# Optimization experiments

Measured on AMD Instinct MI355X. Metric: run time of the kernel, lower is better.

Reference implementation:

```python
import jax, jax.numpy as jnp
import numpy as np

HID = 1024
HEADS = 16
HEAD_DIM = HID // HEADS
FFN = 4096
EPS = 1e-5


def setup_inputs() -> dict:
    key = jax.random.key(0)
    ks = jax.random.split(key, 12)
    s = lambda k, shape, fan_in: jax.random.normal(k, shape, jnp.float32) * (fan_in ** -0.5)
    return {
        "hidden_states": jax.random.normal(ks[0], (2, 2048, HID), jnp.float32),
        "Wq": s(ks[1], (HID, HID), HID),
        "Wk": s(ks[2], (HID, HID), HID),
        "Wv": s(ks[3], (HID, HID), HID),
        "Wo": s(ks[4], (HID, HID), HID),
        "W1": s(ks[5], (HID, FFN), HID),
        "b1": jnp.zeros((FFN,), jnp.float32),
        "W2": s(ks[6], (FFN, HID), FFN),
        "b2": jnp.zeros((HID,), jnp.float32),
        "ln1_scale": jnp.ones((HID,), jnp.float32),
        "ln1_shift": jnp.zeros((HID,), jnp.float32),
        "ln2_scale": jnp.ones((HID,), jnp.float32),
        "ln2_shift": jnp.zeros((HID,), jnp.float32),
    }


def _layer_norm(x, scale, shift):
    mean = jnp.mean(x, axis=-1, keepdims=True)
    var = jnp.var(x, axis=-1, keepdims=True)  # biased, matches unbiased=False
    return (x - mean) * jax.lax.rsqrt(var + EPS) * scale + shift


def _forward(hidden_states, Wq, Wk, Wv, Wo, W1, b1, W2, b2,
             ln1_scale, ln1_shift, ln2_scale, ln2_shift):
    bsz, seq_len, _ = hidden_states.shape
    residual = hidden_states
    x = _layer_norm(hidden_states, ln1_scale, ln1_shift)

    # q/k/v projections -> [b, h, s, d]
    def proj(W):
        return (x @ W).reshape(bsz, seq_len, HEADS, HEAD_DIM).transpose(0, 2, 1, 3)
    q, k, v = proj(Wq), proj(Wk), proj(Wv)

    scores = jnp.einsum("bhqd,bhkd->bhqk", q, k)
    causal = jnp.triu(jnp.ones((seq_len, seq_len), bool), k=1)
    scores = jnp.where(causal, -jnp.inf, scores) / (HEAD_DIM ** 0.5)
    attn = jax.nn.softmax(scores, axis=-1)  # dropout is identity in eval
    out = jnp.einsum("bhqk,bhkd->bhqd", attn, v)
    out = out.transpose(0, 2, 1, 3).reshape(bsz, seq_len, HID)
    hidden_states = residual + out @ Wo

    residual = hidden_states
    y = _layer_norm(hidden_states, ln2_scale, ln2_shift)
    y = jax.nn.gelu(y @ W1 + b1, approximate=False) @ W2 + b2  # torch nn.GELU default = exact erf
    return residual + y


def reference(hidden_states, Wq, Wk, Wv, Wo, W1, b1, W2, b2,
              ln1_scale, ln1_shift, ln2_scale, ln2_shift):
    return _forward(hidden_states, Wq, Wk, Wv, Wo, W1, b1, W2, b2,
                    ln1_scale, ln1_shift, ln2_scale, ln2_shift)
```

## Files before the change

### kernel.cpp

```cpp
#include <hip/hip_runtime.h>
#include <math.h>

using bf16x8 = __attribute__((ext_vector_type(8))) short;
using f32x4  = __attribute__((ext_vector_type(4))) float;

struct __align__(8) us4 { unsigned short x, y, z, w; };
struct __align__(8) u32x2 { unsigned int x, y; };

__device__ __forceinline__ unsigned short f2b(float f) {
  union { float f; unsigned u; } v; v.f = f;
  unsigned r = v.u + 0x7FFFu + ((v.u >> 16) & 1u);
  return (unsigned short)(r >> 16);
}
__device__ __forceinline__ unsigned int cvt_pk_bf16(float lo, float hi) {
  unsigned int d;
  asm("v_cvt_pk_bf16_f32 %0, %1, %2" : "=v"(d) : "v"(lo), "v"(hi));
  return d;
}

#define GLDS(g, l) __builtin_amdgcn_global_load_lds(                        \
    (const __attribute__((address_space(1))) void*)(g),                    \
    (__attribute__((address_space(3))) void*)(l), 16, 0, 0)

__global__ void __launch_bounds__(256) transpose_w(
    const float* __restrict__ src, unsigned short* __restrict__ dst,
    int K, int N) {
  __shared__ float tile[32][33];
  const int n0 = blockIdx.x * 32, k0 = blockIdx.y * 32;
  const int tx = threadIdx.x & 31, ty = threadIdx.x >> 5;
#pragma unroll
  for (int i = 0; i < 32; i += 8)
    tile[ty + i][tx] = src[(size_t)(k0 + ty + i) * N + n0 + tx];
  __syncthreads();
#pragma unroll
  for (int i = 0; i < 32; i += 8)
    dst[(size_t)(n0 + ty + i) * K + k0 + tx] = f2b(tile[tx][ty + i]);
}

__global__ void __launch_bounds__(256) ln_kernel(
    const float* __restrict__ in, const float* __restrict__ scale,
    const float* __restrict__ shift, unsigned short* __restrict__ out) {
  const int row = blockIdx.x, t = threadIdx.x;
  const float4 v = ((const float4*)(in + (size_t)row * 1024))[t];
  float s  = v.x + v.y + v.z + v.w;
  float s2 = v.x * v.x + v.y * v.y + v.z * v.z + v.w * v.w;
#pragma unroll
  for (int off = 32; off; off >>= 1) {
    s  += __shfl_xor(s,  off);
    s2 += __shfl_xor(s2, off);
  }
  __shared__ float red[8];
  const int w = t >> 6, lane = t & 63;
  if (!lane) { red[w] = s; red[4 + w] = s2; }
  __syncthreads();
  s  = red[0] + red[1] + red[2] + red[3];
  s2 = red[4] + red[5] + red[6] + red[7];
  const float mean = s * (1.0f / 1024.0f);
  const float var  = s2 * (1.0f / 1024.0f) - mean * mean;
  const float rstd = rsqrtf(var + 1e-5f);
  const float4 sc = ((const float4*)scale)[t];
  const float4 sh = ((const float4*)shift)[t];
  us4 o;
  o.x = f2b((v.x - mean) * rstd * sc.x + sh.x);
  o.y = f2b((v.y - mean) * rstd * sc.y + sh.y);
  o.z = f2b((v.z - mean) * rstd * sc.z + sh.z);
  o.w = f2b((v.w - mean) * rstd * sc.w + sh.w);
  ((us4*)(out + (size_t)row * 1024))[t] = o;
}

template <int MODE>
__global__ void __launch_bounds__(512, 2) gemm256(
    const unsigned short* __restrict__ A, const unsigned short* __restrict__ B,
    int K, int N, unsigned short* __restrict__ outb,
    const float* __restrict__ bias, unsigned short* __restrict__ vt) {
  __shared__ unsigned short lA[2][256 * 64];
  __shared__ unsigned short lB[2][256 * 64];
  const int t = threadIdx.x, lane = t & 63;
  const int w = t >> 6, wm = w >> 2, wn = w & 3;
  const int r16 = lane & 15, g = lane >> 4;
  const int m0 = blockIdx.x * 256, n0 = blockIdx.y * 256;

  const unsigned short* aSrc[4];
  const unsigned short* bSrc[4];
#pragma unroll
  for (int p = 0; p < 4; ++p) {
    const int ci = t + p * 512, r = ci >> 3, cs = ci & 7;
    aSrc[p] = A + (size_t)(m0 + r) * K + (cs ^ (r & 7)) * 8;
    bSrc[p] = B + (size_t)(n0 + r) * K + (cs ^ (r & 7)) * 8;
  }
  int aOff[8][2], bOff[4][2];
#pragma unroll
  for (int i = 0; i < 8; ++i)
#pragma unroll
    for (int ks = 0; ks < 2; ++ks) {
      const int m = wm * 128 + i * 16 + r16, kb = ks * 4 + g;
      aOff[i][ks] = ((m << 3) + (kb ^ (m & 7))) << 3;
    }
#pragma unroll
  for (int j = 0; j < 4; ++j)
#pragma unroll
    for (int ks = 0; ks < 2; ++ks) {
      const int n = wn * 64 + j * 16 + r16, kb = ks * 4 + g;
      bOff[j][ks] = ((n << 3) + (kb ^ (n & 7))) << 3;
    }

  auto stage = [&](int buf, int kt) {
    const int off = kt * 64;
#pragma unroll
    for (int p = 0; p < 4; ++p) {
      GLDS(aSrc[p] + off, &lA[buf][(t + p * 512) * 8]);
      GLDS(bSrc[p] + off, &lB[buf][(t + p * 512) * 8]);
    }
  };

  f32x4 acc[8][4] = {};
  const int nkt = K >> 6;
  stage(0, 0);
  for (int kt = 0; kt < nkt; ++kt) {
    const int cur = kt & 1;
    if (kt + 1 < nkt) {
      stage(cur ^ 1, kt + 1);
      asm volatile("s_waitcnt vmcnt(8)" ::: "memory");
    } else {
      asm volatile("s_waitcnt vmcnt(0)" ::: "memory");
    }
    __builtin_amdgcn_s_barrier();
    __builtin_amdgcn_sched_barrier(0);
    const unsigned short* bA = lA[cur];
    const unsigned short* bB = lB[cur];
#pragma unroll
    for (int ks = 0; ks < 2; ++ks) {
      bf16x8 af[8], bfr[4];
#pragma unroll
      for (int i = 0; i < 8; ++i) af[i] = *(const bf16x8*)&bA[aOff[i][ks]];
#pragma unroll
      for (int j = 0; j < 4; ++j) bfr[j] = *(const bf16x8*)&bB[bOff[j][ks]];
      __builtin_amdgcn_s_setprio(1);
#pragma unroll
      for (int i = 0; i < 8; ++i)
#pragma unroll
        for (int j = 0; j < 4; ++j)
          acc[i][j] = __builtin_amdgcn_mfma_f32_16x16x32_bf16(
              af[i], bfr[j], acc[i][j], 0, 0, 0);
      __builtin_amdgcn_s_setprio(0);
    }
    __builtin_amdgcn_sched_barrier(0);
    __builtin_amdgcn_s_barrier();
  }

  float bj[4];
  if constexpr (MODE == 2) {
#pragma unroll
    for (int j = 0; j < 4; ++j) bj[j] = bias[n0 + wn * 64 + j * 16 + r16];
  }
#pragma unroll
  for (int i = 0; i < 8; ++i) {
    const int row0 = m0 + wm * 128 + i * 16 + g * 4;
#pragma unroll
    for (int j = 0; j < 4; ++j) {
      const int colb = n0 + wn * 64 + j * 16;
      const int col = colb + r16;
      if constexpr (MODE == 0) {
        if (colb < 2048) {
#pragma unroll
          for (int r = 0; r < 4; ++r)
            outb[(size_t)(row0 + r) * 2048 + col] = f2b(acc[i][j][r]);
        } else {
          const int b = row0 >> 11, s0 = row0 & 2047;
          us4 pk;
          pk.x = f2b(acc[i][j][0]); pk.y = f2b(acc[i][j][1]);
          pk.z = f2b(acc[i][j][2]); pk.w = f2b(acc[i][j][3]);
          *(us4*)&vt[((size_t)b * 1024 + (col - 2048)) * 2048 + s0] = pk;
        }
      } else {
#pragma unroll
        for (int r = 0; r < 4; ++r) {
          const float x = acc[i][j][r] + bj[j];
          const float u = x * (0.7978845608028654f + 0.03567740814f * x * x);
          const float e = __builtin_amdgcn_exp2f(u * 2.885390081777927f);
          const float th = 1.0f - 2.0f * __builtin_amdgcn_rcpf(e + 1.0f);
          outb[(size_t)(row0 + r) * N + col] = f2b(0.5f * x * (1.0f + th));
        }
      }
    }
  }
}

template <int MODE, int BM>
__global__ void __launch_bounds__(256) gemm_bt(
    const unsigned short* __restrict__ A, const unsigned short* __restrict__ B,
    int K, int N,
    float* __restrict__ outf, const float* __restrict__ bias,
    const float* __restrict__ resid) {
  constexpr int WN = (BM == 128) ? 2 : 4;
  constexpr int NJ = 128 / (16 * WN);
  constexpr int ACH = BM / 32;
  __shared__ unsigned short lA[2][BM * 64];
  __shared__ unsigned short lB[2][128 * 64];
  const int t = threadIdx.x, lane = t & 63;
  const int w = t >> 6, wm = w / WN, wn = w % WN;
  const int r16 = lane & 15, g = lane >> 4;
  const int m0 = blockIdx.x * BM, n0 = blockIdx.y * 128;

  const unsigned short* aSrc[ACH];
  const unsigned short* bSrc[4];
#pragma unroll
  for (int p = 0; p < ACH; ++p) {
    const int ci = t + p * 256, m = ci >> 3, cs = ci & 7;
    aSrc[p] = A + (size_t)(m0 + m) * K + (cs ^ (m & 7)) * 8;
  }
#pragma unroll
  for (int p = 0; p < 4; ++p) {
    const int ci = t + p * 256, m = ci >> 3, cs = ci & 7;
    bSrc[p] = B + (size_t)(n0 + m) * K + (cs ^ (m & 7)) * 8;
  }

  int aOff[4][2], bOff[NJ][2];
#pragma unroll
  for (int i = 0; i < 4; ++i)
#pragma unroll
    for (int ks = 0; ks < 2; ++ks) {
      const int m = wm * 64 + i * 16 + r16, kb = ks * 4 + g;
      aOff[i][ks] = ((m << 3) + (kb ^ (m & 7))) << 3;
    }
#pragma unroll
  for (int j = 0; j < NJ; ++j)
#pragma unroll
    for (int ks = 0; ks < 2; ++ks) {
      const int n = wn * (16 * NJ) + j * 16 + r16, kb = ks * 4 + g;
      bOff[j][ks] = ((n << 3) + (kb ^ (n & 7))) << 3;
    }

  auto stage = [&](int buf, int kt) {
    const int off = kt * 64;
#pragma unroll
    for (int p = 0; p < ACH; ++p)
      GLDS(aSrc[p] + off, &lA[buf][(t + p * 256) * 8]);
#pragma unroll
    for (int p = 0; p < 4; ++p)
      GLDS(bSrc[p] + off, &lB[buf][(t + p * 256) * 8]);
  };

  f32x4 acc[4][NJ] = {};
  const int nkt = K >> 6;
  stage(0, 0);
  for (int kt = 0; kt < nkt; ++kt) {
    const int cur = kt & 1;
    if (kt + 1 < nkt) {
      stage(cur ^ 1, kt + 1);
      if constexpr (ACH == 2)
        asm volatile("s_waitcnt vmcnt(6)" ::: "memory");
      else
        asm volatile("s_waitcnt vmcnt(8)" ::: "memory");
    } else {
      asm volatile("s_waitcnt vmcnt(0)" ::: "memory");
    }
    __builtin_amdgcn_s_barrier();
    __builtin_amdgcn_sched_barrier(0);
    const unsigned short* bA = lA[cur];
    const unsigned short* bB = lB[cur];
#pragma unroll
    for (int ks = 0; ks < 2; ++ks) {
      bf16x8 af[4], bfr[NJ];
#pragma unroll
      for (int i = 0; i < 4; ++i) af[i] = *(const bf16x8*)&bA[aOff[i][ks]];
#pragma unroll
      for (int j = 0; j < NJ; ++j) bfr[j] = *(const bf16x8*)&bB[bOff[j][ks]];
      __builtin_amdgcn_s_setprio(1);
#pragma unroll
      for (int i = 0; i < 4; ++i)
#pragma unroll
        for (int j = 0; j < NJ; ++j)
          acc[i][j] = __builtin_amdgcn_mfma_f32_16x16x32_bf16(
              af[i], bfr[j], acc[i][j], 0, 0, 0);
      __builtin_amdgcn_s_setprio(0);
    }
    __builtin_amdgcn_sched_barrier(0);
    __builtin_amdgcn_s_barrier();
  }

  float bj[NJ];
  if constexpr (MODE == 3) {
#pragma unroll
    for (int j = 0; j < NJ; ++j)
      bj[j] = bias[n0 + wn * (16 * NJ) + j * 16 + r16];
  }
#pragma unroll
  for (int i = 0; i < 4; ++i) {
    const int row0 = m0 + wm * 64 + i * 16 + g * 4;
#pragma unroll
    for (int j = 0; j < NJ; ++j) {
      const int col = n0 + wn * (16 * NJ) + j * 16 + r16;
      if constexpr (MODE == 1) {
#pragma unroll
        for (int r = 0; r < 4; ++r) {
          const size_t idx = (size_t)(row0 + r) * N + col;
          outf[idx] = acc[i][j][r] + resid[idx];
        }
      } else {
#pragma unroll
        for (int r = 0; r < 4; ++r) {
          const size_t idx = (size_t)(row0 + r) * N + col;
          outf[idx] = acc[i][j][r] + bj[j] + resid[idx];
        }
      }
    }
  }
}

__global__ void __launch_bounds__(256) attn_kernel(
    const unsigned short* __restrict__ qk, const unsigned short* __restrict__ vt,
    unsigned short* __restrict__ obuf) {
  const int j = blockIdx.x, h = blockIdx.y, bb = blockIdx.z;
  const int t = threadIdx.x, lane = t & 63, w = t >> 6;
  const int r16 = lane & 15, g = lane >> 4;
  __shared__ unsigned short lK[2][64 * 64];
  __shared__ unsigned short lV[2][64 * 64];
  __shared__ unsigned short lP[4][16 * 64];

  const int qtA = j, qtB = 31 - j;
  const int ktmax = qtB;
  const int qrowA = qtA * 64 + w * 16 + r16;
  const int qrowB = qtB * 64 + w * 16 + r16;
  const float CE = 0.18033688011112042f;

  bf16x8 qfA[2], qfB[2];
  {
    const unsigned short* qa = qk + (size_t)(bb * 2048 + qrowA) * 2048 + h * 64;
    qfA[0] = *(const bf16x8*)(qa + g * 8);
    qfA[1] = *(const bf16x8*)(qa + 32 + g * 8);
    const unsigned short* qb = qk + (size_t)(bb * 2048 + qrowB) * 2048 + h * 64;
    qfB[0] = *(const bf16x8*)(qb + g * 8);
    qfB[1] = *(const bf16x8*)(qb + 32 + g * 8);
  }

  f32x4 accA[4] = {}, accB[4] = {};
  float mA = -3.0e38f, lA_ = 0.0f, mB = -3.0e38f, lB_ = 0.0f;

  auto stage = [&](int buf, int kt) {
    const int k0 = kt * 64;
#pragma unroll
    for (int p = 0; p < 2; ++p) {
      const int ci = t + p * 256;
      const int r = ci >> 3, cs = ci & 7;
      const int cb = cs ^ (r & 7);
      GLDS(qk + (size_t)(bb * 2048 + k0 + r) * 2048 + 1024 + h * 64 + cb * 8,
           &lK[buf][ci * 8]);
      GLDS(vt + ((size_t)bb * 1024 + h * 64 + r) * 2048 + k0 + cb * 8,
           &lV[buf][ci * 8]);
    }
  };

  const int pswz = (r16 & 7) << 3;

  auto flash_step = [&](const bf16x8* qf, f32x4* accO, float& mrun,
                        float& lrun, int qrow, bool diag, int k0, int cur) {
    f32x4 s[4] = {};
    __builtin_amdgcn_s_setprio(1);
#pragma unroll
    for (int ks = 0; ks < 2; ++ks)
#pragma unroll
      for (int mt = 0; mt < 4; ++mt) {
        const int r = mt * 16 + r16, db = ks * 4 + g;
        const bf16x8 kf =
            *(const bf16x8*)&lK[cur][((r << 3) + (db ^ (r & 7))) << 3];
        s[mt] = __builtin_amdgcn_mfma_f32_16x16x32_bf16(kf, qf[ks], s[mt],
                                                        0, 0, 0);
      }
    __builtin_amdgcn_s_setprio(0);
    if (diag) {
#pragma unroll
      for (int mt = 0; mt < 4; ++mt)
#pragma unroll
        for (int r = 0; r < 4; ++r)
          if (k0 + mt * 16 + g * 4 + r > qrow) s[mt][r] = -3.0e38f;
    }
    float tmax = -3.0e38f;
#pragma unroll
    for (int mt = 0; mt < 4; ++mt)
#pragma unroll
      for (int r = 0; r < 4; ++r) tmax = fmaxf(tmax, s[mt][r]);
    tmax = fmaxf(tmax, __shfl_xor(tmax, 16));
    tmax = fmaxf(tmax, __shfl_xor(tmax, 32));
    if (!__all(tmax <= mrun + 44.0f)) {
      const float mnew = fmaxf(mrun, tmax);
      const float fac = __builtin_amdgcn_exp2f((mrun - mnew) * CE);
      lrun *= fac;
      float fr[4];
#pragma unroll
      for (int r = 0; r < 4; ++r) fr[r] = __shfl(fac, g * 4 + r);
#pragma unroll
      for (int nb = 0; nb < 4; ++nb)
#pragma unroll
        for (int r = 0; r < 4; ++r) accO[nb][r] *= fr[r];
      mrun = mnew;
    }
    float pv[4][4];
    float tsum = 0.0f;
#pragma unroll
    for (int mt = 0; mt < 4; ++mt)
#pragma unroll
      for (int r = 0; r < 4; ++r) {
        pv[mt][r] = __builtin_amdgcn_exp2f((s[mt][r] - mrun) * CE);
        tsum += pv[mt][r];
      }
    tsum += __shfl_xor(tsum, 16);
    tsum += __shfl_xor(tsum, 32);
    lrun += tsum;
#pragma unroll
    for (int mt = 0; mt < 4; ++mt) {
      u32x2 pk;
      pk.x = cvt_pk_bf16(pv[mt][0], pv[mt][1]);
      pk.y = cvt_pk_bf16(pv[mt][2], pv[mt][3]);
      *(u32x2*)&lP[w][r16 * 64 + ((mt * 16 + g * 4) ^ pswz)] = pk;
    }
    __builtin_amdgcn_s_setprio(1);
#pragma unroll
    for (int ks = 0; ks < 2; ++ks) {
      const bf16x8 pa =
          *(const bf16x8*)&lP[w][r16 * 64 + ((ks * 32 + g * 8) ^ pswz)];
#pragma unroll
      for (int nb = 0; nb < 4; ++nb) {
        const int d = nb * 16 + r16, kb = ks * 4 + g;
        const bf16x8 vf =
            *(const bf16x8*)&lV[cur][((d << 3) + (kb ^ (d & 7))) << 3];
        accO[nb] = __builtin_amdgcn_mfma_f32_16x16x32_bf16(pa, vf, accO[nb],
                                                           0, 0, 0);
      }
    }
    __builtin_amdgcn_s_setprio(0);
  };

  stage(0, 0);
  __syncthreads();
  int cur = 0;
  for (int kt = 0; kt <= ktmax; ++kt) {
    if (kt < ktmax) stage(cur ^ 1, kt + 1);
    flash_step(qfB, accB, mB, lB_, qrowB, kt == qtB, kt * 64, cur);
    if (kt <= qtA)
      flash_step(qfA, accA, mA, lA_, qrowA, kt == qtA, kt * 64, cur);
    __syncthreads();
    cur ^= 1;
  }

  auto epilogue = [&](const f32x4* accO, float lrun, int q0) {
    const float li = 1.0f / lrun;
    float lr_[4];
#pragma unroll
    for (int r = 0; r < 4; ++r) lr_[r] = __shfl(li, g * 4 + r);
#pragma unroll
    for (int nb = 0; nb < 4; ++nb)
#pragma unroll
      for (int r = 0; r < 4; ++r) {
        const int row = bb * 2048 + q0 + w * 16 + g * 4 + r;
        const int col = h * 64 + nb * 16 + r16;
        obuf[(size_t)row * 1024 + col] = f2b(accO[nb][r] * lr_[r]);
      }
  };
  epilogue(accA, lA_, qtA * 64);
  epilogue(accB, lB_, qtB * 64);
}

extern "C" void kernel_launch(void* const* d_in, const int* in_sizes, int n_in,
                              void* d_out, int out_size, void* d_ws,
                              size_t ws_size, hipStream_t stream) {
  const float* hs   = (const float*)d_in[0];
  const float* Wq   = (const float*)d_in[1];
  const float* Wk   = (const float*)d_in[2];
  const float* Wv   = (const float*)d_in[3];
  const float* Wo   = (const float*)d_in[4];
  const float* W1   = (const float*)d_in[5];
  const float* b1   = (const float*)d_in[6];
  const float* W2   = (const float*)d_in[7];
  const float* b2   = (const float*)d_in[8];
  const float* ln1s = (const float*)d_in[9];
  const float* ln1b = (const float*)d_in[10];
  const float* ln2s = (const float*)d_in[11];
  const float* ln2b = (const float*)d_in[12];
  float* out = (float*)d_out;

  char* ws = (char*)d_ws;
  unsigned short* wqkvT = (unsigned short*)(ws + 0);
  unsigned short* woT   = (unsigned short*)(ws + 6291456);
  unsigned short* w1T   = (unsigned short*)(ws + 8388608);
  unsigned short* w2T   = (unsigned short*)(ws + 16777216);
  float*          hid   = (float*)(ws + 25165824);
  unsigned short* xb    = (unsigned short*)(ws + 41943040);
  char*           big   = ws + 50331648;
  unsigned short* qkb   = (unsigned short*)(big);
  unsigned short* vtb   = (unsigned short*)(big + 16777216);
  unsigned short* ob    = (unsigned short*)(big + 25165824);
  unsigned short* h1    = (unsigned short*)(big);

  transpose_w<<<dim3(32, 32), 256, 0, stream>>>(Wq, wqkvT, 1024, 1024);
  transpose_w<<<dim3(32, 32), 256, 0, stream>>>(Wk, wqkvT + 1024 * 1024, 1024, 1024);
  transpose_w<<<dim3(32, 32), 256, 0, stream>>>(Wv, wqkvT + 2 * 1024 * 1024, 1024, 1024);
  transpose_w<<<dim3(32, 32), 256, 0, stream>>>(Wo, woT, 1024, 1024);
  transpose_w<<<dim3(128, 32), 256, 0, stream>>>(W1, w1T, 1024, 4096);
  transpose_w<<<dim3(32, 128), 256, 0, stream>>>(W2, w2T, 4096, 1024);

  ln_kernel<<<4096, 256, 0, stream>>>(hs, ln1s, ln1b, xb);
  gemm256<0><<<dim3(16, 12), 512, 0, stream>>>(xb, wqkvT, 1024, 3072,
                                               qkb, nullptr, vtb);
  attn_kernel<<<dim3(16, 16, 2), 256, 0, stream>>>(qkb, vtb, ob);
  gemm_bt<1, 64><<<dim3(64, 8), 256, 0, stream>>>(ob, woT, 1024, 1024,
                                                  hid, nullptr, hs);
  ln_kernel<<<4096, 256, 0, stream>>>(hid, ln2s, ln2b, xb);
  gemm256<2><<<dim3(16, 16), 512, 0, stream>>>(xb, w1T, 1024, 4096,
                                               h1, b1, nullptr);
  gemm_bt<3, 64><<<dim3(64, 8), 256, 0, stream>>>(h1, w2T, 4096, 1024,
                                                  out, b2, hid);
}
```

Baseline: 242.7 us.

## Split GEMM k-step into half-tile phases and remap blocks across XCDs

Each 64-wide k-tile in the 256x256 GEMM is now split into four phases: half of the A fragments are read with the B fragments, MFMAs run, then the other half of A is read. Workgroup barriers between phases keep the waves in step, and fewer fragment registers are live at once. Block indices are also remapped so consecutive tiles land on the same XCD chiplet, which is meant to improve L2 reuse. The extra barriers and lgkmcnt(0) waits may serialize LDS reads against MFMA work and reduce overlap. The remap assumes the block count divides by 8.

```diff
diff --git a/kernel.cpp b/kernel.cpp
--- a/kernel.cpp
+++ b/kernel.cpp
@@ -78,7 +78,10 @@
   const int t = threadIdx.x, lane = t & 63;
   const int w = t >> 6, wm = w >> 2, wn = w & 3;
   const int r16 = lane & 15, g = lane >> 4;
-  const int m0 = blockIdx.x * 256, n0 = blockIdx.y * 256;
+  const int gx = gridDim.x, nwg = gx * gridDim.y;
+  const int fb = blockIdx.y * gx + blockIdx.x;
+  const int sb = (fb & 7) * (nwg >> 3) + (fb >> 3);
+  const int m0 = (sb % gx) * 256, n0 = (sb / gx) * 256;
 
   const unsigned short* aSrc[4];
   const unsigned short* bSrc[4];
@@ -128,20 +131,67 @@
     __builtin_amdgcn_sched_barrier(0);
     const unsigned short* bA = lA[cur];
     const unsigned short* bB = lB[cur];
-#pragma unroll
-    for (int ks = 0; ks < 2; ++ks) {
-      bf16x8 af[8], bfr[4];
-#pragma unroll
-      for (int i = 0; i < 8; ++i) af[i] = *(const bf16x8*)&bA[aOff[i][ks]];
-#pragma unroll
-      for (int j = 0; j < 4; ++j) bfr[j] = *(const bf16x8*)&bB[bOff[j][ks]];
+
+    bf16x8 af[4], bfr[4];
+#pragma unroll
+    for (int i = 0; i < 4; ++i) af[i] = *(const bf16x8*)&bA[aOff[i][0]];
+#pragma unroll
+    for (int j = 0; j < 4; ++j) bfr[j] = *(const bf16x8*)&bB[bOff[j][0]];
+    asm volatile("s_waitcnt lgkmcnt(0)" ::: "memory");
+    __builtin_amdgcn_sched_barrier(0);
+    __builtin_amdgcn_s_setprio(1);
+#pragma unroll
+    for (int i = 0; i < 4; ++i)
+#pragma unroll
+      for (int j = 0; j < 4; ++j)
+        acc[i][j] = __builtin_amdgcn_mfma_f32_16x16x32_bf16(
+            af[i], bfr[j], acc[i][j], 0, 0, 0);
+    __builtin_amdgcn_s_setprio(0);
+    __builtin_amdgcn_s_barrier();
+    {
+      bf16x8 a2[4];
+#pragma unroll
+      for (int i = 0; i < 4; ++i) a2[i] = *(const bf16x8*)&bA[aOff[4 + i][0]];
+      asm volatile("s_waitcnt lgkmcnt(0)" ::: "memory");
+      __builtin_amdgcn_sched_barrier(0);
       __builtin_amdgcn_s_setprio(1);
 #pragma unroll
-      for (int i = 0; i < 8; ++i)
+      for (int i = 0; i < 4; ++i)
 #pragma unroll
         for (int j = 0; j < 4; ++j)
-          acc[i][j] = __builtin_amdgcn_mfma_f32_16x16x32_bf16(
-              af[i], bfr[j], acc[i][j], 0, 0, 0);
+          acc[4 + i][j] = __builtin_amdgcn_mfma_f32_16x16x32_bf16(
+              a2[i], bfr[j], acc[4 + i][j], 0, 0, 0);
+      __builtin_amdgcn_s_setprio(0);
+    }
+    __builtin_amdgcn_s_barrier();
+#pragma unroll
+    for (int i = 0; i < 4; ++i) af[i] = *(const bf16x8*)&bA[aOff[i][1]];
+#pragma unroll
+    for (int j = 0; j < 4; ++j) bfr[j] = *(const bf16x8*)&bB[bOff[j][1]];
+    asm volatile("s_waitcnt lgkmcnt(0)" ::: "memory");
+    __builtin_amdgcn_sched_barrier(0);
+    __builtin_amdgcn_s_setprio(1);
+#pragma unroll
+    for (int i = 0; i < 4; ++i)
+#pragma unroll
+      for (int j = 0; j < 4; ++j)
+        acc[i][j] = __builtin_amdgcn_mfma_f32_16x16x32_bf16(
+            af[i], bfr[j], acc[i][j], 0, 0, 0);
+    __builtin_amdgcn_s_setprio(0);
+    __builtin_amdgcn_s_barrier();
+    {
+      bf16x8 a2[4];
+#pragma unroll
+      for (int i = 0; i < 4; ++i) a2[i] = *(const bf16x8*)&bA[aOff[4 + i][1]];
+      asm volatile("s_waitcnt lgkmcnt(0)" ::: "memory");
+      __builtin_amdgcn_sched_barrier(0);
+      __builtin_amdgcn_s_setprio(1);
+#pragma unroll
+      for (int i = 0; i < 4; ++i)
+#pragma unroll
+        for (int j = 0; j < 4; ++j)
+          acc[4 + i][j] = __builtin_amdgcn_mfma_f32_16x16x32_bf16(
+              a2[i], bfr[j], acc[4 + i][j], 0, 0, 0);
       __builtin_amdgcn_s_setprio(0);
     }
     __builtin_amdgcn_sched_barrier(0);
```

New measurement: 247.9 us. +2.1%, slower.

## Fuse weight transposes with LN1 and widen attention KV tiles to 128

Applied to the files above, without the earlier changes.

The six weight-transpose launches and the first layernorm are merged into one prep kernel that dispatches on block index, removing several kernel launches and their tail gaps. The attention kernel now stages 128-key K/V tiles per iteration instead of 64. That halves the number of loop iterations and barriers and gives more MFMA work between syncs. In exchange, LDS use per block roughly doubles, which may lower occupancy, and the causal diagonal tile now wastes more masked work.

```diff
diff --git a/kernel.cpp b/kernel.cpp
--- a/kernel.cpp
+++ b/kernel.cpp
@@ -22,12 +22,65 @@
     (const __attribute__((address_space(1))) void*)(g),                    \
     (__attribute__((address_space(3))) void*)(l), 16, 0, 0)
 
-__global__ void __launch_bounds__(256) transpose_w(
-    const float* __restrict__ src, unsigned short* __restrict__ dst,
-    int K, int N) {
+__global__ void __launch_bounds__(256) prep_kernel(
+    const float* __restrict__ hs, const float* __restrict__ ln1s,
+    const float* __restrict__ ln1b, unsigned short* __restrict__ xb,
+    const float* __restrict__ Wq, const float* __restrict__ Wk,
+    const float* __restrict__ Wv, const float* __restrict__ Wo,
+    const float* __restrict__ W1, const float* __restrict__ W2,
+    unsigned short* __restrict__ wqkvT, unsigned short* __restrict__ woT,
+    unsigned short* __restrict__ w1T, unsigned short* __restrict__ w2T) {
+  const int id = blockIdx.x;
+  const int t = threadIdx.x;
   __shared__ float tile[32][33];
-  const int n0 = blockIdx.x * 32, k0 = blockIdx.y * 32;
-  const int tx = threadIdx.x & 31, ty = threadIdx.x >> 5;
+  __shared__ float red[8];
+
+  if (id < 4096) {
+    const int row = id;
+    const float4 v = ((const float4*)(hs + (size_t)row * 1024))[t];
+    float s  = v.x + v.y + v.z + v.w;
+    float s2 = v.x * v.x + v.y * v.y + v.z * v.z + v.w * v.w;
+#pragma unroll
+    for (int off = 32; off; off >>= 1) {
+      s  += __shfl_xor(s,  off);
+      s2 += __shfl_xor(s2, off);
+    }
+    const int w = t >> 6, lane = t & 63;
+    if (!lane) { red[w] = s; red[4 + w] = s2; }
+    __syncthreads();
+    s  = red[0] + red[1] + red[2] + red[3];
+    s2 = red[4] + red[5] + red[6] + red[7];
+    const float mean = s * (1.0f / 1024.0f);
+    const float var  = s2 * (1.0f / 1024.0f) - mean * mean;
+    const float rstd = rsqrtf(var + 1e-5f);
+    const float4 sc = ((const float4*)ln1s)[t];
+    const float4 sh = ((const float4*)ln1b)[t];
+    us4 o;
+    o.x = f2b((v.x - mean) * rstd * sc.x + sh.x);
+    o.y = f2b((v.y - mean) * rstd * sc.y + sh.y);
+    o.z = f2b((v.z - mean) * rstd * sc.z + sh.z);
+    o.w = f2b((v.w - mean) * rstd * sc.w + sh.w);
+    ((us4*)(xb + (size_t)row * 1024))[t] = o;
+    return;
+  }
+
+  const float* src; unsigned short* dst; int K, N, n0, k0;
+  if (id < 8192) {
+    const int which = (id - 4096) >> 10, local = (id - 4096) & 1023;
+    src = (which == 0) ? Wq : (which == 1) ? Wk : (which == 2) ? Wv : Wo;
+    dst = (which == 3) ? woT : wqkvT + (size_t)which * 1048576;
+    K = 1024; N = 1024;
+    n0 = (local & 31) * 32; k0 = (local >> 5) * 32;
+  } else if (id < 12288) {
+    const int local = id - 8192;
+    src = W1; dst = w1T; K = 1024; N = 4096;
+    n0 = (local & 127) * 32; k0 = (local >> 7) * 32;
+  } else {
+    const int local = id - 12288;
+    src = W2; dst = w2T; K = 4096; N = 1024;
+    n0 = (local & 31) * 32; k0 = (local >> 5) * 32;
+  }
+  const int tx = t & 31, ty = t >> 5;
 #pragma unroll
   for (int i = 0; i < 32; i += 8)
     tile[ty + i][tx] = src[(size_t)(k0 + ty + i) * N + n0 + tx];
@@ -314,12 +367,12 @@
   const int j = blockIdx.x, h = blockIdx.y, bb = blockIdx.z;
   const int t = threadIdx.x, lane = t & 63, w = t >> 6;
   const int r16 = lane & 15, g = lane >> 4;
-  __shared__ unsigned short lK[2][64 * 64];
-  __shared__ unsigned short lV[2][64 * 64];
-  __shared__ unsigned short lP[4][16 * 64];
+  __shared__ unsigned short lK[2][128 * 64];
+  __shared__ unsigned short lV[2][64 * 128];
+  __shared__ unsigned short lP[4][16 * 128];
 
   const int qtA = j, qtB = 31 - j;
-  const int ktmax = qtB;
+  const int ktA = qtA >> 1, ktB = qtB >> 1;
   const int qrowA = qtA * 64 + w * 16 + r16;
   const int qrowB = qtB * 64 + w * 16 + r16;
   const float CE = 0.18033688011112042f;
@@ -338,15 +391,17 @@
   float mA = -3.0e38f, lA_ = 0.0f, mB = -3.0e38f, lB_ = 0.0f;
 
   auto stage = [&](int buf, int kt) {
-    const int k0 = kt * 64;
-#pragma unroll
-    for (int p = 0; p < 2; ++p) {
+    const int k0 = kt * 128;
+#pragma unroll
+    for (int p = 0; p < 4; ++p) {
       const int ci = t + p * 256;
       const int r = ci >> 3, cs = ci & 7;
-      const int cb = cs ^ (r & 7);
-      GLDS(qk + (size_t)(bb * 2048 + k0 + r) * 2048 + 1024 + h * 64 + cb * 8,
+      GLDS(qk + (size_t)(bb * 2048 + k0 + r) * 2048 + 1024 + h * 64 +
+               (cs ^ (r & 7)) * 8,
            &lK[buf][ci * 8]);
-      GLDS(vt + ((size_t)bb * 1024 + h * 64 + r) * 2048 + k0 + cb * 8,
+      const int r2 = ci >> 4, cs2 = ci & 15;
+      GLDS(vt + ((size_t)bb * 1024 + h * 64 + r2) * 2048 + k0 +
+               (cs2 ^ (r2 & 7)) * 8,
            &lV[buf][ci * 8]);
     }
   };
@@ -355,12 +410,12 @@
 
   auto flash_step = [&](const bf16x8* qf, f32x4* accO, float& mrun,
                         float& lrun, int qrow, bool diag, int k0, int cur) {
-    f32x4 s[4] = {};
+    f32x4 s[8] = {};
     __builtin_amdgcn_s_setprio(1);
 #pragma unroll
     for (int ks = 0; ks < 2; ++ks)
 #pragma unroll
-      for (int mt = 0; mt < 4; ++mt) {
+      for (int mt = 0; mt < 8; ++mt) {
         const int r = mt * 16 + r16, db = ks * 4 + g;
         const bf16x8 kf =
             *(const bf16x8*)&lK[cur][((r << 3) + (db ^ (r & 7))) << 3];
@@ -370,14 +425,14 @@
     __builtin_amdgcn_s_setprio(0);
     if (diag) {
 #pragma unroll
-      for (int mt = 0; mt < 4; ++mt)
+      for (int mt = 0; mt < 8; ++mt)
 #pragma unroll
         for (int r = 0; r < 4; ++r)
           if (k0 + mt * 16 + g * 4 + r > qrow) s[mt][r] = -3.0e38f;
     }
     float tmax = -3.0e38f;
 #pragma unroll
-    for (int mt = 0; mt < 4; ++mt)
+    for (int mt = 0; mt < 8; ++mt)
 #pragma unroll
       for (int r = 0; r < 4; ++r) tmax = fmaxf(tmax, s[mt][r]);
     tmax = fmaxf(tmax, __shfl_xor(tmax, 16));
@@ -395,35 +450,33 @@
         for (int r = 0; r < 4; ++r) accO[nb][r] *= fr[r];
       mrun = mnew;
     }
-    float pv[4][4];
     float tsum = 0.0f;
 #pragma unroll
-    for (int mt = 0; mt < 4; ++mt)
+    for (int mt = 0; mt < 8; ++mt) {
+      float pv[4];
 #pragma unroll
       for (int r = 0; r < 4; ++r) {
-        pv[mt][r] = __builtin_amdgcn_exp2f((s[mt][r] - mrun) * CE);
-        tsum += pv[mt][r];
+        pv[r] = __builtin_amdgcn_exp2f((s[mt][r] - mrun) * CE);
+        tsum += pv[r];
       }
+      u32x2 pk;
+      pk.x = cvt_pk_bf16(pv[0], pv[1]);
+      pk.y = cvt_pk_bf16(pv[2], pv[3]);
+      *(u32x2*)&lP[w][r16 * 128 + ((mt * 16 + g * 4) ^ pswz)] = pk;
+    }
     tsum += __shfl_xor(tsum, 16);
     tsum += __shfl_xor(tsum, 32);
     lrun += tsum;
-#pragma unroll
-    for (int mt = 0; mt < 4; ++mt) {
-      u32x2 pk;
-      pk.x = cvt_pk_bf16(pv[mt][0], pv[mt][1]);
-      pk.y = cvt_pk_bf16(pv[mt][2], pv[mt][3]);
-      *(u32x2*)&lP[w][r16 * 64 + ((mt * 16 + g * 4) ^ pswz)] = pk;
-    }
     __builtin_amdgcn_s_setprio(1);
 #pragma unroll
-    for (int ks = 0; ks < 2; ++ks) {
+    for (int ks = 0; ks < 4; ++ks) {
       const bf16x8 pa =
-          *(const bf16x8*)&lP[w][r16 * 64 + ((ks * 32 + g * 8) ^ pswz)];
+          *(const bf16x8*)&lP[w][r16 * 128 + ((ks * 32 + g * 8) ^ pswz)];
 #pragma unroll
       for (int nb = 0; nb < 4; ++nb) {
         const int d = nb * 16 + r16, kb = ks * 4 + g;
         const bf16x8 vf =
-            *(const bf16x8*)&lV[cur][((d << 3) + (kb ^ (d & 7))) << 3];
+            *(const bf16x8*)&lV[cur][((d << 4) + (kb ^ (d & 7))) << 3];
         accO[nb] = __builtin_amdgcn_mfma_f32_16x16x32_bf16(pa, vf, accO[nb],
                                                            0, 0, 0);
       }
@@ -434,11 +487,11 @@
   stage(0, 0);
   __syncthreads();
   int cur = 0;
-  for (int kt = 0; kt <= ktmax; ++kt) {
-    if (kt < ktmax) stage(cur ^ 1, kt + 1);
-    flash_step(qfB, accB, mB, lB_, qrowB, kt == qtB, kt * 64, cur);
-    if (kt <= qtA)
-      flash_step(qfA, accA, mA, lA_, qrowA, kt == qtA, kt * 64, cur);
+  for (int kt = 0; kt <= ktB; ++kt) {
+    if (kt < ktB) stage(cur ^ 1, kt + 1);
+    flash_step(qfB, accB, mB, lB_, qrowB, kt == ktB, kt * 128, cur);
+    if (kt <= ktA)
+      flash_step(qfA, accA, mA, lA_, qrowA, kt == ktA, kt * 128, cur);
     __syncthreads();
     cur ^= 1;
   }
@@ -492,14 +545,9 @@
   unsigned short* ob    = (unsigned short*)(big + 25165824);
   unsigned short* h1    = (unsigned short*)(big);
 
-  transpose_w<<<dim3(32, 32), 256, 0, stream>>>(Wq, wqkvT, 1024, 1024);
-  transpose_w<<<dim3(32, 32), 256, 0, stream>>>(Wk, wqkvT + 1024 * 1024, 1024, 1024);
-  transpose_w<<<dim3(32, 32), 256, 0, stream>>>(Wv, wqkvT + 2 * 1024 * 1024, 1024, 1024);
-  transpose_w<<<dim3(32, 32), 256, 0, stream>>>(Wo, woT, 1024, 1024);
-  transpose_w<<<dim3(128, 32), 256, 0, stream>>>(W1, w1T, 1024, 4096);
-  transpose_w<<<dim3(32, 128), 256, 0, stream>>>(W2, w2T, 4096, 1024);
-
-  ln_kernel<<<4096, 256, 0, stream>>>(hs, ln1s, ln1b, xb);
+  prep_kernel<<<16384, 256, 0, stream>>>(hs, ln1s, ln1b, xb,
+                                         Wq, Wk, Wv, Wo, W1, W2,
+                                         wqkvT, woT, w1T, w2T);
   gemm256<0><<<dim3(16, 12), 512, 0, stream>>>(xb, wqkvT, 1024, 3072,
                                                qkb, nullptr, vtb);
   attn_kernel<<<dim3(16, 16, 2), 256, 0, stream>>>(qkb, vtb, ob);
```

Result: slower. 249.7 us (+2.9%).
